# Kernel optimization log

Hardware: AMD Instinct MI355X
Metric: run time of the kernel (lower is better)

## Reference

```python
import jax, jax.numpy as jnp
import numpy as np

B, N, C, KV = 4, 4096, 1024, 1024
H = 4            # hardcoded 4-way split in the source
Ch, Kh = C // H, KV // H
EPS = 1e-5       # InstanceNorm2d default eps


def setup_inputs() -> dict:
    key = jax.random.key(0)
    ks = jax.random.split(key, 12)
    s = 0.02
    return {
        "emb1":     jax.random.normal(ks[0], (B, N, C),  jnp.float32),
        "emb_all":  jax.random.normal(ks[1], (B, N, KV), jnp.float32),
        "embd1":    jax.random.normal(ks[2], (B, N, C),  jnp.float32),
        "emb_alld": jax.random.normal(ks[3], (B, N, KV), jnp.float32),
        # per-head query weights (distinct per split), torch Linear layout [out,in]
        "Wq":   jax.random.normal(ks[4],  (H, Ch, Ch), jnp.float32) * s,
        "Wqd":  jax.random.normal(ks[5],  (H, Ch, Ch), jnp.float32) * s,
        # source reuses key[0]/value[0] for all splits -> single shared weight
        "Wk0":  jax.random.normal(ks[6],  (Kh, Kh), jnp.float32) * s,
        "Wv0":  jax.random.normal(ks[7],  (Kh, Kh), jnp.float32) * s,
        "Wkd0": jax.random.normal(ks[8],  (Kh, Kh), jnp.float32) * s,
        "Wvd0": jax.random.normal(ks[9],  (Kh, Kh), jnp.float32) * s,
        "Wout":  jax.random.normal(ks[10], (C, C), jnp.float32) * s,
        "Woutd": jax.random.normal(ks[11], (C, C), jnp.float32) * s,
    }


def _inorm(s):
    # InstanceNorm2d(affine=False): normalize over the (C/4, KV/4) plane per (b, head)
    m = s.mean(axis=(2, 3), keepdims=True)
    v = ((s - m) ** 2).mean(axis=(2, 3), keepdims=True)
    return (s - m) * jax.lax.rsqrt(v + EPS)


def reference(emb1, emb_all, embd1, emb_alld,
              Wq, Wqd, Wk0, Wv0, Wkd0, Wvd0, Wout, Woutd):
    scale = 1.0 / np.sqrt(KV).astype(np.float32)
    # split into 4 channel groups and project (Q: per-group weight; K/V: shared weight)
    Q  = jnp.einsum('bnhc,hoc->bhno', emb1.reshape(B, N, H, Ch),  Wq)    # [B,H,N,Ch]
    Qd = jnp.einsum('bnhc,hoc->bhno', embd1.reshape(B, N, H, Ch), Wqd)
    K  = jnp.einsum('bnhk,ok->bhno', emb_all.reshape(B, N, H, Kh),  Wk0)  # [B,H,N,Kh]
    V  = jnp.einsum('bnhk,ok->bhno', emb_all.reshape(B, N, H, Kh),  Wv0)
    Kd = jnp.einsum('bnhk,ok->bhno', emb_alld.reshape(B, N, H, Kh), Wkd0)
    Vd = jnp.einsum('bnhk,ok->bhno', emb_alld.reshape(B, N, H, Kh), Wvd0)
    # channel-attention scores: contract over tokens N -> [B,H,Ch,Kh]
    s1  = jnp.einsum('bhnc,bhnk->bhck', Q,  Kd) * scale
    sd1 = jnp.einsum('bhnc,bhnk->bhck', Qd, K)  * scale
    p1  = jax.nn.softmax(_inorm(s1),  axis=-1)
    pd1 = jax.nn.softmax(_inorm(sd1), axis=-1)
    # context: probs @ V^T -> [b,h,c,n]; permute(0,3,2,1)+view -> [B,N,C] (c-major, h-minor)
    ctx1  = jnp.einsum('bhck,bhnk->bnch', p1,  Vd).reshape(B, N, C)
    ctxd1 = jnp.einsum('bhck,bhnk->bnch', pd1, V ).reshape(B, N, C)
    O1  = ctx1  @ Wout.T
    Od1 = ctxd1 @ Woutd.T
    return (O1, Od1)
```

## Files before the change

kernel.cpp:

```cpp
#include <hip/hip_runtime.h>
#include <math.h>


#define PITCH 40

typedef __bf16 bf16x4 __attribute__((ext_vector_type(4)));
typedef __bf16 bf16x8 __attribute__((ext_vector_type(8)));
typedef float f32x4 __attribute__((ext_vector_type(4)));

__device__ inline void gl2lds16(const void* g, void* l) {
    __builtin_amdgcn_global_load_lds(
        (const __attribute__((address_space(1))) unsigned int*)g,
        (__attribute__((address_space(3))) unsigned int*)l, 16, 0, 0);
}

__global__ __launch_bounds__(256) void prep_x(const float* __restrict__ emb_all,
                                              const float* __restrict__ emb_alld,
                                              __bf16* __restrict__ Xb) {
    const float* src = blockIdx.y ? emb_alld : emb_all;
    __bf16* dst = Xb + (long long)blockIdx.y * 16777216;
    long long i4 = (long long)blockIdx.x * 256 + threadIdx.x;
    float4 v = *(const float4*)&src[i4 * 4];
    bf16x4 o = {(__bf16)v.x, (__bf16)v.y, (__bf16)v.z, (__bf16)v.w};
    *(bf16x4*)&dst[i4 * 4] = o;
}

__global__ __launch_bounds__(256) void prep_w(
    const float* __restrict__ Wq, const float* __restrict__ Wqd,
    const float* __restrict__ Wk0, const float* __restrict__ Wv0,
    const float* __restrict__ Wkd0, const float* __restrict__ Wvd0,
    const float* __restrict__ Wout, const float* __restrict__ Woutd,
    __bf16* __restrict__ Wq_bf, __bf16* __restrict__ Wk_bf,
    __bf16* __restrict__ WvT_bf, __bf16* __restrict__ WoutR_bf)
{
    int id = blockIdx.x * 256 + threadIdx.x;
    if (id < 524288) {
        Wq_bf[id] = (__bf16)(id < 262144 ? Wq[id] : Wqd[id - 262144]);
    } else if (id < 655360) {
        int j = id - 524288;
        Wk_bf[j] = (__bf16)(j < 65536 ? Wkd0[j] : Wk0[j - 65536]);
    } else if (id < 786432) {
        int j = id - 655360;
        int p = j >> 16, r = (j >> 8) & 255, c2 = j & 255;
        const float* s = p ? Wv0 : Wvd0;
        WvT_bf[j] = (__bf16)s[c2 * 256 + r];
    } else if (id < 2883584) {
        int j = id - 786432;
        int p = j >> 20; int rem = j & 1048575; int h = rem >> 18; int oc = rem & 262143;
        int o = oc >> 8, c = oc & 255;
        const float* s = p ? Woutd : Wout;
        WoutR_bf[j] = (__bf16)s[o * 1024 + c * 4 + h];
    }
}

__global__ __launch_bounds__(256) void gram_mfma(
    const float* __restrict__ emb1, const float* __restrict__ emb_all,
    const float* __restrict__ embd1, const float* __restrict__ emb_alld,
    float* __restrict__ Gpart)
{
    __shared__ __bf16 As[128 * PITCH];
    __shared__ __bf16 Bs[128 * PITCH];

    const int z = blockIdx.z;
    const int path = z >> 4, bh = z & 15;
    const int b = bh >> 2, h = bh & 3;
    const float* Xm = (path == 0 ? emb_alld : emb_all) + (long long)b * 4194304 + h * 256;
    const float* Xn = (path == 0 ? emb1     : embd1)   + (long long)b * 4194304 + h * 256;

    const int i0 = (blockIdx.x >> 1) * 128;
    const int j0 = (blockIdx.x & 1) * 128;
    const int kb0 = blockIdx.y * 1024;

    const int t = threadIdx.x;
    const int q  = t & 7;
    const int i4 = t >> 3;
    const int lane = t & 63;
    const int wave = t >> 6;
    const int wr = (wave >> 1) * 64, wc = (wave & 1) * 64;
    const int fm = lane & 15, fg = lane >> 4;

    f32x4 acc[4][4];
#pragma unroll
    for (int u = 0; u < 4; ++u)
#pragma unroll
        for (int v = 0; v < 4; ++v) acc[u][v] = (f32x4){0.f, 0.f, 0.f, 0.f};

    for (int kb = kb0; kb < kb0 + 1024; kb += 32) {
        float4 va[4], vb[4];
        const float* pa = Xm + (long long)(kb + q * 4) * 1024 + i0 + i4 * 4;
        const float* pb = Xn + (long long)(kb + q * 4) * 1024 + j0 + i4 * 4;
#pragma unroll
        for (int r = 0; r < 4; ++r) {
            va[r] = *(const float4*)(pa + (long long)r * 1024);
            vb[r] = *(const float4*)(pb + (long long)r * 1024);
        }
        __syncthreads();
#pragma unroll
        for (int c = 0; c < 4; ++c) {
            bf16x4 wa, wb;
#pragma unroll
            for (int r = 0; r < 4; ++r) {
                wa[r] = (__bf16)(((const float*)&va[r])[c]);
                wb[r] = (__bf16)(((const float*)&vb[r])[c]);
            }
            *(bf16x4*)&As[(i4 * 4 + c) * PITCH + q * 4] = wa;
            *(bf16x4*)&Bs[(i4 * 4 + c) * PITCH + q * 4] = wb;
        }
        __syncthreads();

        bf16x8 af[4], bfv[4];
#pragma unroll
        for (int mt = 0; mt < 4; ++mt)
            af[mt] = *(const bf16x8*)&As[(wr + mt * 16 + fm) * PITCH + fg * 8];
#pragma unroll
        for (int nt = 0; nt < 4; ++nt)
            bfv[nt] = *(const bf16x8*)&Bs[(wc + nt * 16 + fm) * PITCH + fg * 8];
#pragma unroll
        for (int mt = 0; mt < 4; ++mt)
#pragma unroll
            for (int nt = 0; nt < 4; ++nt)
                acc[mt][nt] = __builtin_amdgcn_mfma_f32_16x16x32_bf16(af[mt], bfv[nt], acc[mt][nt], 0, 0, 0);
    }

    float* Gp = Gpart + ((long long)blockIdx.y * 32 + z) * 65536;
    const int col = lane & 15, rq = (lane >> 4) * 4;
#pragma unroll
    for (int mt = 0; mt < 4; ++mt)
#pragma unroll
        for (int nt = 0; nt < 4; ++nt)
#pragma unroll
            for (int r = 0; r < 4; ++r)
                Gp[(i0 + wr + mt * 16 + rq + r) * 256 + (j0 + wc + nt * 16 + col)] = acc[mt][nt][r];
}

__global__ __launch_bounds__(256) void reduce_g(const float* __restrict__ Gpart, __bf16* __restrict__ GT) {
    long long idx4 = (long long)blockIdx.x * 256 + threadIdx.x;
    float4 a = *(const float4*)&Gpart[idx4 * 4];
    float4 b = *(const float4*)&Gpart[2097152 + idx4 * 4];
    float4 c = *(const float4*)&Gpart[4194304 + idx4 * 4];
    float4 d = *(const float4*)&Gpart[6291456 + idx4 * 4];
    bf16x4 o;
    o[0] = (__bf16)(a.x + b.x + c.x + d.x);
    o[1] = (__bf16)(a.y + b.y + c.y + d.y);
    o[2] = (__bf16)(a.z + b.z + c.z + d.z);
    o[3] = (__bf16)(a.w + b.w + c.w + d.w);
    *(bf16x4*)&GT[idx4 * 4] = o;
}

template <typename CT>
__global__ __launch_bounds__(256) void mfma_nt(
    const __bf16* __restrict__ A, const __bf16* __restrict__ B, CT* __restrict__ C,
    int mtiles, int K,
    long long a1, long long a2, long long a3,
    long long b1, long long b2, long long b3,
    long long c1, long long c2, long long c3,
    int cpitch, float alpha)
{
    __shared__ __bf16 As[64 * 32];
    __shared__ __bf16 Bs[64 * 32];
    const int z = blockIdx.y;
    const __bf16* Az = A + (long long)(z >> 4) * a1 + (long long)((z >> 2) & 3) * a2 + (long long)(z & 3) * a3;
    const __bf16* Bz = B + (long long)(z >> 4) * b1 + (long long)((z >> 2) & 3) * b2 + (long long)(z & 3) * b3;
    CT* Cz = C + (long long)(z >> 4) * c1 + (long long)((z >> 2) & 3) * c2 + (long long)(z & 3) * c3;

    const int tm = blockIdx.x % mtiles, tn = blockIdx.x / mtiles;
    const int t = threadIdx.x;
    const int lane = t & 63, wave = t >> 6;
    const int row = t >> 2, ch = t & 3;
    const int fm = lane & 15, fg = lane >> 4;

    const __bf16* ga = Az + (long long)(tm * 64 + row) * K + ch * 8;
    const __bf16* gb = Bz + (long long)(tn * 64 + row) * K + ch * 8;
    __bf16* la = &As[t * 8];
    __bf16* lb = &Bs[t * 8];

    f32x4 acc[4];
#pragma unroll
    for (int u = 0; u < 4; ++u) acc[u] = (f32x4){0.f, 0.f, 0.f, 0.f};

    for (int kb = 0; kb < K; kb += 32) {
        __syncthreads();
        gl2lds16(ga + kb, la);
        gl2lds16(gb + kb, lb);
        __syncthreads();
        bf16x8 bv = *(const bf16x8*)&Bs[(wave * 16 + fm) * 32 + fg * 8];
#pragma unroll
        for (int mt = 0; mt < 4; ++mt) {
            bf16x8 av = *(const bf16x8*)&As[(mt * 16 + fm) * 32 + fg * 8];
            acc[mt] = __builtin_amdgcn_mfma_f32_16x16x32_bf16(av, bv, acc[mt], 0, 0, 0);
        }
    }

    const int colc = tn * 64 + wave * 16 + fm;
    const int rq = fg * 4;
#pragma unroll
    for (int mt = 0; mt < 4; ++mt)
#pragma unroll
        for (int r = 0; r < 4; ++r) {
            int rowc = tm * 64 + mt * 16 + rq + r;
            Cz[(long long)rowc * cpitch + colc] = (CT)(acc[mt][r] * alpha);
        }
}


#define VMCNT4 asm volatile("s_waitcnt vmcnt(4)" ::: "memory")
#define VMCNT2 asm volatile("s_waitcnt vmcnt(2)" ::: "memory")
#define VMCNT0 asm volatile("s_waitcnt vmcnt(0)" ::: "memory")
#define BARR   asm volatile("s_barrier" ::: "memory")

#define STAGE_A(h, kt, c) do { \
    _Pragma("unroll") \
    for (int o = 0; o < 2; ++o) { \
        int rl = (h) * 64 + o * 128 + stg_row; \
        gl2lds16(Xa + (long long)rl * 1024 + (kt) * 64 + stg_col, \
                 &lds[(c) * 32768 + rl * 64 + lin_col]); \
    } \
} while (0)

#define STAGE_B(h, kt, c) do { \
    _Pragma("unroll") \
    for (int o = 0; o < 2; ++o) { \
        int rl = o * 128 + (h) * 32 + (stg_row & 31) + ((stg_row & 32) << 1); \
        gl2lds16(Bb + (long long)rl * 1024 + (kt) * 64 + stg_col, \
                 &lds[(c) * 32768 + 16384 + rl * 64 + lin_col]); \
    } \
} while (0)

#define LOAD_A(hm, c) do { \
    _Pragma("unroll") \
    for (int mt = 0; mt < 4; ++mt) { \
        const __bf16* p = &lds[(c) * 32768 + (wr * 128 + (hm) * 64 + mt * 16 + fm) * 64]; \
        af[mt][0] = *(const bf16x8*)&p[(fg * 8) ^ rsw]; \
        af[mt][1] = *(const bf16x8*)&p[(32 + fg * 8) ^ rsw]; \
    } \
} while (0)

#define LOAD_B(hn, c) do { \
    _Pragma("unroll") \
    for (int nt = 0; nt < 2; ++nt) { \
        const __bf16* p = &lds[(c) * 32768 + 16384 + (wc * 64 + (hn) * 32 + nt * 16 + fm) * 64]; \
        bv[(hn) * 2 + nt][0] = *(const bf16x8*)&p[(fg * 8) ^ rsw]; \
        bv[(hn) * 2 + nt][1] = *(const bf16x8*)&p[(32 + fg * 8) ^ rsw]; \
    } \
} while (0)

#define MFMA_Q(hm, hn) do { \
    __builtin_amdgcn_s_setprio(1); \
    _Pragma("unroll") \
    for (int mt = 0; mt < 4; ++mt) \
        _Pragma("unroll") \
        for (int nt = 0; nt < 2; ++nt) { \
            acc[(hm) * 4 + mt][(hn) * 2 + nt] = __builtin_amdgcn_mfma_f32_16x16x32_bf16( \
                af[mt][0], bv[(hn) * 2 + nt][0], acc[(hm) * 4 + mt][(hn) * 2 + nt], 0, 0, 0); \
            acc[(hm) * 4 + mt][(hn) * 2 + nt] = __builtin_amdgcn_mfma_f32_16x16x32_bf16( \
                af[mt][1], bv[(hn) * 2 + nt][1], acc[(hm) * 4 + mt][(hn) * 2 + nt], 0, 0, 0); \
        } \
    __builtin_amdgcn_s_setprio(0); \
} while (0)

__global__ __launch_bounds__(512, 2) void obig8(
    const __bf16* __restrict__ Xall, const __bf16* __restrict__ Mb, float* __restrict__ out)
{
    __shared__ __bf16 lds[65536];

    const int id = blockIdx.x;
    const int wg = (id & 7) * 64 + (id >> 3);
    const int z = wg >> 6;
    const int tile = wg & 63;
    const int tm = tile & 15, tn = tile >> 4;
    const int path = z >> 2, b = z & 3;

    const __bf16* Xa = Xall + (path == 0 ? 16777216LL : 0LL)
                     + (long long)b * 4194304 + (long long)tm * 262144;
    const __bf16* Bb = Mb + (long long)path * 4194304 + (long long)b * 1048576
                     + (long long)tn * 262144;
    float* Ob = out + (long long)path * 16777216 + (long long)b * 4194304;

    const int t = threadIdx.x;
    const int lane = t & 63, wave = t >> 6;
    const int wr = wave >> 2, wc = wave & 3;
    const int fm = lane & 15, fg = lane >> 4;
    const int stg_row = t >> 3;
    const int lin_col = (t & 7) * 8;
    const int stg_col = ((t & 7) ^ (stg_row & 7)) * 8;
    const int rsw = (fm & 7) * 8;

    f32x4 acc[8][4];
#pragma unroll
    for (int u = 0; u < 8; ++u)
#pragma unroll
        for (int v = 0; v < 4; ++v) acc[u][v] = (f32x4){0.f, 0.f, 0.f, 0.f};

    bf16x8 af[4][2];
    bf16x8 bv[8][2];

    STAGE_A(0, 0, 0);
    STAGE_B(0, 0, 0);
    STAGE_B(1, 0, 0);
    STAGE_A(1, 0, 0);
    VMCNT4;
    BARR;

    for (int kt = 0; kt < 15; ++kt) {
        const int c = kt & 1, n = c ^ 1;
        LOAD_A(0, c);
        LOAD_B(0, c);
        STAGE_A(0, kt + 1, n);
        VMCNT4;
        BARR;
        MFMA_Q(0, 0);
        BARR;
        LOAD_B(1, c);
        STAGE_B(0, kt + 1, n);
        VMCNT4;
        BARR;
        MFMA_Q(0, 1);
        BARR;
        LOAD_A(1, c);
        STAGE_B(1, kt + 1, n);
        BARR;
        MFMA_Q(1, 1);
        BARR;
        STAGE_A(1, kt + 1, n);
        VMCNT4;
        BARR;
        MFMA_Q(1, 0);
        BARR;
    }

    {
        LOAD_A(0, 1);
        LOAD_B(0, 1);
        VMCNT2;
        BARR;
        MFMA_Q(0, 0);
        BARR;
        LOAD_B(1, 1);
        VMCNT0;
        BARR;
        MFMA_Q(0, 1);
        BARR;
        LOAD_A(1, 1);
        MFMA_Q(1, 1);
        MFMA_Q(1, 0);
    }

    const int rq = fg * 4;
    float* op = Ob + (long long)(tm * 256 + wr * 128 + rq) * 1024 + tn * 256 + wc * 64 + fm;
#pragma unroll
    for (int mi = 0; mi < 8; ++mi)
#pragma unroll
        for (int ni = 0; ni < 4; ++ni)
#pragma unroll
            for (int r = 0; r < 4; ++r)
                op[(long long)(mi * 16 + r) * 1024 + ni * 16] = acc[mi][ni][r];
}

__global__ __launch_bounds__(256) void stats_kernel(const float* __restrict__ S, float* __restrict__ st) {
    int pg = blockIdx.x;
    const float* s = S + (long long)pg * 65536;
    float sum = 0.f, sq = 0.f;
    for (int i = threadIdx.x; i < 65536; i += 256) {
        float v = s[i];
        sum += v;
        sq += v * v;
    }
#pragma unroll
    for (int off = 32; off; off >>= 1) {
        sum += __shfl_down(sum, off);
        sq  += __shfl_down(sq,  off);
    }
    __shared__ float r1[4], r2[4];
    int w = threadIdx.x >> 6;
    if ((threadIdx.x & 63) == 0) { r1[w] = sum; r2[w] = sq; }
    __syncthreads();
    if (threadIdx.x == 0) {
        float ts = r1[0] + r1[1] + r1[2] + r1[3];
        float tq = r2[0] + r2[1] + r2[2] + r2[3];
        float mean = ts * (1.0f / 65536.0f);
        float var = tq * (1.0f / 65536.0f) - mean * mean;
        st[pg * 2 + 0] = mean;
        st[pg * 2 + 1] = rsqrtf(var + 1e-5f);
    }
}

__global__ __launch_bounds__(256) void softmax_kernel(const float* __restrict__ S,
                                                      const float* __restrict__ st,
                                                      __bf16* __restrict__ p_bf) {
    int pg = blockIdx.y;
    int c = blockIdx.x;
    float mean = st[pg * 2 + 0], rstd = st[pg * 2 + 1];
    const float* row = S + (long long)pg * 65536 + c * 256;
    int t = threadIdx.x;
    float x = (row[t] - mean) * rstd;
    float m = x;
#pragma unroll
    for (int off = 32; off; off >>= 1) m = fmaxf(m, __shfl_down(m, off));
    __shared__ float r1[4], r2[4];
    int w = t >> 6;
    if ((t & 63) == 0) r1[w] = m;
    __syncthreads();
    m = fmaxf(fmaxf(r1[0], r1[1]), fmaxf(r1[2], r1[3]));
    float e = expf(x - m);
    float ssum = e;
#pragma unroll
    for (int off = 32; off; off >>= 1) ssum += __shfl_down(ssum, off);
    if ((t & 63) == 0) r2[w] = ssum;
    __syncthreads();
    ssum = r2[0] + r2[1] + r2[2] + r2[3];
    p_bf[(long long)pg * 65536 + c * 256 + t] = (__bf16)(e / ssum);
}

extern "C" void kernel_launch(void* const* d_in, const int* in_sizes, int n_in,
                              void* d_out, int out_size, void* d_ws, size_t ws_size,
                              hipStream_t stream) {
    const float* emb1     = (const float*)d_in[0];
    const float* emb_all  = (const float*)d_in[1];
    const float* embd1    = (const float*)d_in[2];
    const float* emb_alld = (const float*)d_in[3];
    const float* Wq    = (const float*)d_in[4];
    const float* Wqd   = (const float*)d_in[5];
    const float* Wk0   = (const float*)d_in[6];
    const float* Wv0   = (const float*)d_in[7];
    const float* Wkd0  = (const float*)d_in[8];
    const float* Wvd0  = (const float*)d_in[9];
    const float* Wout  = (const float*)d_in[10];
    const float* Woutd = (const float*)d_in[11];
    float* out = (float*)d_out;

    float* ws = (float*)d_ws;
    float*  Gpart   = ws;
    __bf16* Mb_bf   = (__bf16*)ws;
    __bf16* X_bf    = (__bf16*)(ws + 8388608);
    __bf16* GT_bf   = (__bf16*)(ws + 25165824);
    __bf16* T_bf    = (__bf16*)(ws + 26214400);
    float*  S       = ws + 27262976;
    __bf16* p_bf    = (__bf16*)(ws + 29360128);
    __bf16* PT_bf   = (__bf16*)(ws + 30408704);
    __bf16* Wq_bf   = (__bf16*)(ws + 31457280);
    __bf16* Wk_bf   = (__bf16*)(ws + 31719424);
    __bf16* WvT_bf  = (__bf16*)(ws + 31784960);
    __bf16* WoutR_bf= (__bf16*)(ws + 31850496);
    float*  st      = ws + 32899072;

    dim3 blk(256);

    prep_x<<<dim3(16384, 2), blk, 0, stream>>>(emb_all, emb_alld, X_bf);
    prep_w<<<11264, blk, 0, stream>>>(Wq, Wqd, Wk0, Wv0, Wkd0, Wvd0, Wout, Woutd,
                                      Wq_bf, Wk_bf, WvT_bf, WoutR_bf);

    gram_mfma<<<dim3(4, 4, 32), blk, 0, stream>>>(emb1, emb_all, embd1, emb_alld, Gpart);
    reduce_g<<<2048, blk, 0, stream>>>(Gpart, GT_bf);

    mfma_nt<__bf16><<<dim3(16, 32), blk, 0, stream>>>(
        Wq_bf, GT_bf, T_bf, 4, 256,
        262144, 0, 65536,  1048576, 262144, 65536,  1048576, 262144, 65536, 256, 1.0f);
    mfma_nt<float><<<dim3(16, 32), blk, 0, stream>>>(
        T_bf, Wk_bf, S, 4, 256,
        1048576, 262144, 65536,  65536, 0, 0,  1048576, 262144, 65536, 256, 0.03125f);

    stats_kernel<<<32, blk, 0, stream>>>(S, st);
    softmax_kernel<<<dim3(256, 32), blk, 0, stream>>>(S, st, p_bf);

    mfma_nt<__bf16><<<dim3(16, 32), blk, 0, stream>>>(
        WvT_bf, p_bf, PT_bf, 4, 256,
        65536, 0, 0,  1048576, 262144, 65536,  1048576, 262144, 65536, 256, 1.0f);
    mfma_nt<__bf16><<<dim3(64, 32), blk, 0, stream>>>(
        WoutR_bf, PT_bf, Mb_bf, 16, 256,
        1048576, 0, 262144,  1048576, 262144, 65536,  4194304, 1048576, 256, 1024, 1.0f);

    obig8<<<dim3(512), dim3(512), 0, stream>>>(X_bf, Mb_bf, out);
}
```

Baseline: 568.9 us.

## Deepen GEMM global-to-LDS prefetch to two k-tiles ahead

Restructures the main bf16 GEMM mainloop so the global_load_lds staging runs two k-tiles ahead instead of one. Both LDS buffers are filled in the prologue, and each iteration refills the buffer it is currently consuming, after the matching fragments have been read into registers. The wait counters are relaxed to vmcnt(8) to cover more loads in flight, and the tail is split into two drain iterations. The aim is to hide more global memory latency behind MFMA work. The cost is tighter reasoning about when an LDS buffer can safely be overwritten relative to the barriers.

```diff
diff --git a/kernel.cpp b/kernel.cpp
--- a/kernel.cpp
+++ b/kernel.cpp
@@ -203,8 +203,7 @@
 }
 
 
-#define VMCNT4 asm volatile("s_waitcnt vmcnt(4)" ::: "memory")
-#define VMCNT2 asm volatile("s_waitcnt vmcnt(2)" ::: "memory")
+#define VMCNT8 asm volatile("s_waitcnt vmcnt(8)" ::: "memory")
 #define VMCNT0 asm volatile("s_waitcnt vmcnt(0)" ::: "memory")
 #define BARR   asm volatile("s_barrier" ::: "memory")
 
@@ -294,35 +293,51 @@
     bf16x8 af[4][2];
     bf16x8 bv[8][2];
 
-    STAGE_A(0, 0, 0);
-    STAGE_B(0, 0, 0);
-    STAGE_B(1, 0, 0);
-    STAGE_A(1, 0, 0);
-    VMCNT4;
+    STAGE_A(0, 0, 0); STAGE_B(0, 0, 0); STAGE_B(1, 0, 0); STAGE_A(1, 0, 0);
+    STAGE_A(0, 1, 1); STAGE_B(0, 1, 1); STAGE_B(1, 1, 1); STAGE_A(1, 1, 1);
+    VMCNT8;
     BARR;
 
-    for (int kt = 0; kt < 15; ++kt) {
-        const int c = kt & 1, n = c ^ 1;
+    for (int kt = 0; kt < 14; ++kt) {
+        const int c = kt & 1;
         LOAD_A(0, c);
         LOAD_B(0, c);
-        STAGE_A(0, kt + 1, n);
-        VMCNT4;
         BARR;
         MFMA_Q(0, 0);
         BARR;
         LOAD_B(1, c);
-        STAGE_B(0, kt + 1, n);
-        VMCNT4;
+        STAGE_A(0, kt + 2, c);
         BARR;
         MFMA_Q(0, 1);
         BARR;
         LOAD_A(1, c);
-        STAGE_B(1, kt + 1, n);
+        STAGE_B(0, kt + 2, c);
         BARR;
         MFMA_Q(1, 1);
         BARR;
-        STAGE_A(1, kt + 1, n);
-        VMCNT4;
+        STAGE_B(1, kt + 2, c);
+        STAGE_A(1, kt + 2, c);
+        VMCNT8;
+        BARR;
+        MFMA_Q(1, 0);
+        BARR;
+    }
+
+    {
+        LOAD_A(0, 0);
+        LOAD_B(0, 0);
+        BARR;
+        MFMA_Q(0, 0);
+        BARR;
+        LOAD_B(1, 0);
+        BARR;
+        MFMA_Q(0, 1);
+        BARR;
+        LOAD_A(1, 0);
+        BARR;
+        MFMA_Q(1, 1);
+        BARR;
+        VMCNT0;
         BARR;
         MFMA_Q(1, 0);
         BARR;
@@ -331,15 +346,9 @@
     {
         LOAD_A(0, 1);
         LOAD_B(0, 1);
-        VMCNT2;
-        BARR;
         MFMA_Q(0, 0);
-        BARR;
         LOAD_B(1, 1);
-        VMCNT0;
-        BARR;
         MFMA_Q(0, 1);
-        BARR;
         LOAD_A(1, 1);
         MFMA_Q(1, 1);
         MFMA_Q(1, 0);
```

Result: no change. 567.9 us (-0.2%).
